# Performance work log

Hardware: AMD Instinct MI355X
Metric: run time of the kernel (lower is better)

The kernel has to match this reference:

```python
import jax, jax.numpy as jnp
import numpy as np

TOP_K = 5  # top_k_actions from __init__
EPS = 1e-10


def setup_inputs() -> dict:
    key = jax.random.key(0)
    k1, k2, k3 = jax.random.split(key, 3)
    B, A, D2 = 32, 2048, 2048  # batch, num candidate actions, 2*D embed dim
    s_embed = jax.random.normal(k1, (B, D2), dtype=jnp.float32)
    a_embeds_target = jax.random.normal(k2, (B, A, D2), dtype=jnp.float32)
    available_mask = jax.random.randint(k3, (B, A), 0, 2).astype(jnp.bool_)
    alpha = jnp.ones((1,), dtype=jnp.float32)
    return {
        "s_embed": s_embed,
        "a_embeds_target": a_embeds_target,
        "available_mask": available_mask,
        "alpha": alpha,
    }


def _top_mask(logits, k):
    # torch.topk -> scatter True at top-k indices along action dim
    B, A = logits.shape
    _, ids = jax.lax.top_k(logits, k)  # [B, k]
    mask = jnp.zeros((B, A), dtype=jnp.bool_)
    return mask.at[jnp.arange(B)[:, None], ids].set(True)


def _masked_logsumexp(x, mask):
    # matches torch logsumexp helper: unmasked max for stabilization,
    # masked exp-sum, clamp(min=1e-10)
    s = jnp.max(x, axis=-1, keepdims=True)
    exp_x = jnp.exp(x - s) * mask.astype(x.dtype)
    out = s + jnp.log(jnp.clip(jnp.sum(exp_x, axis=-1, keepdims=True), EPS))
    return out[..., 0]


def reference(s_embed, a_embeds_target, available_mask, alpha):
    B, A = available_mask.shape
    D = s_embed.shape[-1] // 2
    alpha = alpha[0]
    # dual-head dot products: [B, 1, D] * [B, A, D] -> [B, A]
    logits_1 = jnp.einsum('bd,bad->ba', s_embed[:, :D], a_embeds_target[:, :, :D])
    logits_2 = jnp.einsum('bd,bad->ba', s_embed[:, D:], a_embeds_target[:, :, D:])
    k = min(A, TOP_K)
    m1 = available_mask & _top_mask(logits_1, k)
    m2 = available_mask & _top_mask(logits_2, k)
    v1 = alpha * _masked_logsumexp(logits_1 / alpha, m1)
    v2 = alpha * _masked_logsumexp(logits_2 / alpha, m2)
    return (v1, v2)
```

## Files before the change

kernel.cpp:

```cpp
#include <hip/hip_runtime.h>
#include <math.h>

#define BATCH 32
#define NACT  2048
#define DIM2  2048
#define TOPK  5

#define ACTIONS_PER_BLOCK 32

__global__ __launch_bounds__(256) void logits_kernel(
    const float* __restrict__ s_embed,
    const float* __restrict__ a_emb,
    float* __restrict__ logits)
{
    const int tile  = blockIdx.x;
    const int b     = tile / (NACT / ACTIONS_PER_BLOCK);
    const int a0    = (tile % (NACT / ACTIONS_PER_BLOCK)) * ACTIONS_PER_BLOCK;
    const int wave  = threadIdx.x >> 6;
    const int lane  = threadIdx.x & 63;

    float4 sreg[8];
    const float* srow = s_embed + (size_t)b * DIM2 + lane * 4;
    #pragma unroll
    for (int i = 0; i < 8; ++i)
        sreg[i] = *(const float4*)(srow + 256 * i);

    const int APW = ACTIONS_PER_BLOCK / 4;
    for (int j = 0; j < APW; ++j) {
        const int a = a0 + wave * APW + j;
        const float* p = a_emb + ((size_t)b * NACT + a) * DIM2 + lane * 4;
        float d1 = 0.f, d2 = 0.f;
        #pragma unroll
        for (int i = 0; i < 4; ++i) {
            float4 v = *(const float4*)(p + 256 * i);
            d1 += v.x * sreg[i].x + v.y * sreg[i].y + v.z * sreg[i].z + v.w * sreg[i].w;
        }
        #pragma unroll
        for (int i = 4; i < 8; ++i) {
            float4 v = *(const float4*)(p + 256 * i);
            d2 += v.x * sreg[i].x + v.y * sreg[i].y + v.z * sreg[i].z + v.w * sreg[i].w;
        }
        #pragma unroll
        for (int off = 32; off >= 1; off >>= 1) {
            d1 += __shfl_xor(d1, off, 64);
            d2 += __shfl_xor(d2, off, 64);
        }
        if (lane == 0) {
            logits[(size_t)b * NACT + a]                         = d1;
            logits[(size_t)BATCH * NACT + (size_t)b * NACT + a]  = d2;
        }
    }
}

__global__ __launch_bounds__(256) void topk_lse_kernel(
    const float* __restrict__ logits,
    const int* __restrict__ avail,
    const float* __restrict__ alpha_p,
    float* __restrict__ out)
{
    __shared__ float xs[NACT];
    __shared__ float sval[256];
    __shared__ int   sidx[256];
    __shared__ float smax, ssum;

    const int h = blockIdx.x / BATCH;
    const int b = blockIdx.x % BATCH;
    const int t = threadIdx.x;

    const float* row = logits + ((size_t)h * BATCH + b) * NACT;
    for (int i = t; i < NACT; i += 256) xs[i] = row[i];
    if (t == 0) ssum = 0.f;
    __syncthreads();

    const float alpha = alpha_p[0];

    for (int it = 0; it < TOPK; ++it) {
        float best = -INFINITY; int bi = NACT;
        for (int i = t; i < NACT; i += 256) {
            float v = xs[i];
            if (v > best) { best = v; bi = i; }
        }
        sval[t] = best; sidx[t] = bi;
        __syncthreads();
        for (int stride = 128; stride >= 1; stride >>= 1) {
            if (t < stride) {
                float v2 = sval[t + stride]; int i2 = sidx[t + stride];
                if (v2 > sval[t] || (v2 == sval[t] && i2 < sidx[t])) {
                    sval[t] = v2; sidx[t] = i2;
                }
            }
            __syncthreads();
        }
        if (t == 0) {
            float v = sval[0]; int idx = sidx[0];
            if (it == 0) smax = v;
            if (avail[(size_t)b * NACT + idx])
                ssum += expf((v - smax) / alpha);
            xs[idx] = -INFINITY;
        }
        __syncthreads();
    }

    if (t == 0) {
        float sum = fmaxf(ssum, 1e-10f);
        out[h * BATCH + b] = smax + alpha * logf(sum);
    }
}

extern "C" void kernel_launch(void* const* d_in, const int* in_sizes, int n_in,
                              void* d_out, int out_size, void* d_ws, size_t ws_size,
                              hipStream_t stream) {
    const float* s_embed = (const float*)d_in[0];
    const float* a_emb   = (const float*)d_in[1];
    const int*   avail   = (const int*)d_in[2];
    const float* alpha   = (const float*)d_in[3];
    float*       out     = (float*)d_out;
    float*       logits  = (float*)d_ws;

    logits_kernel<<<BATCH * (NACT / ACTIONS_PER_BLOCK), 256, 0, stream>>>(
        s_embed, a_emb, logits);
    topk_lse_kernel<<<2 * BATCH, 256, 0, stream>>>(logits, avail, alpha, out);
}
```

Measured before the change: 694.9 us.

## Unroll action loop with batched reductions and use wave-per-row top-k

```diff
diff --git a/kernel.cpp b/kernel.cpp
--- a/kernel.cpp
+++ b/kernel.cpp
@@ -5,8 +5,8 @@
 #define NACT  2048
 #define DIM2  2048
 #define TOPK  5
-
 #define ACTIONS_PER_BLOCK 32
+#define APW   8
 
 __global__ __launch_bounds__(256) void logits_kernel(
     const float* __restrict__ s_embed,
@@ -14,8 +14,8 @@
     float* __restrict__ logits)
 {
     const int tile  = blockIdx.x;
-    const int b     = tile / (NACT / ACTIONS_PER_BLOCK);
-    const int a0    = (tile % (NACT / ACTIONS_PER_BLOCK)) * ACTIONS_PER_BLOCK;
+    const int b     = tile >> 6;
+    const int a0    = (tile & 63) * ACTIONS_PER_BLOCK;
     const int wave  = threadIdx.x >> 6;
     const int lane  = threadIdx.x & 63;
 
@@ -25,10 +25,13 @@
     for (int i = 0; i < 8; ++i)
         sreg[i] = *(const float4*)(srow + 256 * i);
 
-    const int APW = ACTIONS_PER_BLOCK / 4;
+    const int abase = a0 + wave * APW;
+    const float* pbase = a_emb + ((size_t)b * NACT + abase) * DIM2 + lane * 4;
+
+    float acc1[APW], acc2[APW];
+    #pragma unroll
     for (int j = 0; j < APW; ++j) {
-        const int a = a0 + wave * APW + j;
-        const float* p = a_emb + ((size_t)b * NACT + a) * DIM2 + lane * 4;
+        const float* p = pbase + (size_t)j * DIM2;
         float d1 = 0.f, d2 = 0.f;
         #pragma unroll
         for (int i = 0; i < 4; ++i) {
@@ -40,15 +43,24 @@
             float4 v = *(const float4*)(p + 256 * i);
             d2 += v.x * sreg[i].x + v.y * sreg[i].y + v.z * sreg[i].z + v.w * sreg[i].w;
         }
+        acc1[j] = d1;
+        acc2[j] = d2;
+    }
+
+    #pragma unroll
+    for (int off = 32; off >= 1; off >>= 1) {
         #pragma unroll
-        for (int off = 32; off >= 1; off >>= 1) {
-            d1 += __shfl_xor(d1, off, 64);
-            d2 += __shfl_xor(d2, off, 64);
+        for (int j = 0; j < APW; ++j) {
+            acc1[j] += __shfl_xor(acc1[j], off, 64);
+            acc2[j] += __shfl_xor(acc2[j], off, 64);
         }
-        if (lane == 0) {
-            logits[(size_t)b * NACT + a]                         = d1;
-            logits[(size_t)BATCH * NACT + (size_t)b * NACT + a]  = d2;
-        }
+    }
+
+    if (lane == 0) {
+        float* o1 = logits + (size_t)b * NACT + abase;
+        float* o2 = o1 + (size_t)BATCH * NACT;
+        #pragma unroll
+        for (int j = 0; j < APW; ++j) { o1[j] = acc1[j]; o2[j] = acc2[j]; }
     }
 }
 
@@ -58,53 +70,41 @@
     const float* __restrict__ alpha_p,
     float* __restrict__ out)
 {
-    __shared__ float xs[NACT];
-    __shared__ float sval[256];
-    __shared__ int   sidx[256];
-    __shared__ float smax, ssum;
+    const int row  = blockIdx.x * 4 + (threadIdx.x >> 6);
+    const int lane = threadIdx.x & 63;
+    const int b    = row & 31;
 
-    const int h = blockIdx.x / BATCH;
-    const int b = blockIdx.x % BATCH;
-    const int t = threadIdx.x;
-
-    const float* row = logits + ((size_t)h * BATCH + b) * NACT;
-    for (int i = t; i < NACT; i += 256) xs[i] = row[i];
-    if (t == 0) ssum = 0.f;
-    __syncthreads();
+    const float* x = logits + (size_t)row * NACT;
+    float v[32];
+    #pragma unroll
+    for (int k = 0; k < 32; ++k) v[k] = x[k * 64 + lane];
 
     const float alpha = alpha_p[0];
+    float smax = 0.f, ssum = 0.f;
 
     for (int it = 0; it < TOPK; ++it) {
-        float best = -INFINITY; int bi = NACT;
-        for (int i = t; i < NACT; i += 256) {
-            float v = xs[i];
-            if (v > best) { best = v; bi = i; }
+        float best = -INFINITY; int bi = 1 << 30;
+        #pragma unroll
+        for (int k = 0; k < 32; ++k) {
+            float val = v[k];
+            if (val > best) { best = val; bi = k * 64 + lane; }
         }
-        sval[t] = best; sidx[t] = bi;
-        __syncthreads();
-        for (int stride = 128; stride >= 1; stride >>= 1) {
-            if (t < stride) {
-                float v2 = sval[t + stride]; int i2 = sidx[t + stride];
-                if (v2 > sval[t] || (v2 == sval[t] && i2 < sidx[t])) {
-                    sval[t] = v2; sidx[t] = i2;
-                }
-            }
-            __syncthreads();
+        #pragma unroll
+        for (int off = 32; off >= 1; off >>= 1) {
+            float v2 = __shfl_xor(best, off, 64);
+            int   i2 = __shfl_xor(bi,   off, 64);
+            if (v2 > best || (v2 == best && i2 < bi)) { best = v2; bi = i2; }
         }
-        if (t == 0) {
-            float v = sval[0]; int idx = sidx[0];
-            if (it == 0) smax = v;
-            if (avail[(size_t)b * NACT + idx])
-                ssum += expf((v - smax) / alpha);
-            xs[idx] = -INFINITY;
-        }
-        __syncthreads();
+        if (it == 0) smax = best;
+        if (avail[(size_t)b * NACT + bi])
+            ssum += expf((best - smax) / alpha);
+        #pragma unroll
+        for (int k = 0; k < 32; ++k)
+            if (k * 64 + lane == bi) v[k] = -INFINITY;
     }
 
-    if (t == 0) {
-        float sum = fmaxf(ssum, 1e-10f);
-        out[h * BATCH + b] = smax + alpha * logf(sum);
-    }
+    if (lane == 0)
+        out[row] = smax + alpha * logf(fmaxf(ssum, 1e-10f));
 }
 
 extern "C" void kernel_launch(void* const* d_in, const int* in_sizes, int n_in,
@@ -119,5 +119,5 @@
 
     logits_kernel<<<BATCH * (NACT / ACTIONS_PER_BLOCK), 256, 0, stream>>>(
         s_embed, a_emb, logits);
-    topk_lse_kernel<<<2 * BATCH, 256, 0, stream>>>(logits, avail, alpha, out);
+    topk_lse_kernel<<<16, 256, 0, stream>>>(logits, avail, alpha, out);
 }
```

After: 683.6 us. Within noise of the previous version (-1.6%).
